# Kernel tuning notes

Hardware: AMD Instinct MI355X
Metric: run time of the kernel (lower is better)

The kernel has to match this reference:

```python
import jax, jax.numpy as jnp
import numpy as np

N = 20000   # nodes
E = 320000  # edges (before self-loops)
D = 128     # hidden_dim (= per-head out channels, concat=False)
H = 4       # heads
NEG_SLOPE = 0.2   # GATv2 leaky_relu default
LN_EPS = 1e-5


def setup_inputs() -> dict:
    key = jax.random.key(0)
    ks = jax.random.split(key, 12)
    s = 0.05
    w = lambda k, shp: (jax.random.normal(k, shp, jnp.float32) * s)
    return {
        "x": jax.random.normal(ks[0], (N, D), jnp.float32),
        "src": jax.random.randint(ks[1], (E,), 0, N, jnp.int32),
        "dst": jax.random.randint(ks[2], (E,), 0, N, jnp.int32),
        "Wl1": w(ks[3], (D, H * D)), "Wr1": w(ks[4], (D, H * D)),
        "att1": w(ks[5], (H, D)), "b1": jnp.zeros((D,), jnp.float32),
        "g1": jnp.ones((D,), jnp.float32), "be1": jnp.zeros((D,), jnp.float32),
        "Wl2": w(ks[6], (D, H * D)), "Wr2": w(ks[7], (D, H * D)),
        "att2": w(ks[8], (H, D)), "b2": jnp.zeros((D,), jnp.float32),
        "g2": jnp.ones((D,), jnp.float32), "be2": jnp.zeros((D,), jnp.float32),
    }


def gatv2_conv(x, src, dst, Wl, Wr, att, bias):
    """GATv2Conv with concat=False (mean over heads), share_weights=False."""
    n = x.shape[0]
    xl = (x @ Wl).reshape(n, H, D)  # source-side projection
    xr = (x @ Wr).reshape(n, H, D)  # target-side projection
    m = jax.nn.leaky_relu(xl[src] + xr[dst], NEG_SLOPE)     # [E', H, D]
    e = jnp.einsum('ehd,hd->eh', m, att)                     # [E', H]
    # segment softmax over edges grouped by destination node
    e_max = jax.ops.segment_max(e, dst, num_segments=n)      # [N, H]
    ex = jnp.exp(e - e_max[dst])
    denom = jax.ops.segment_sum(ex, dst, num_segments=n)     # [N, H]
    alpha = ex / (denom[dst] + 1e-16)                        # [E', H]
    out = jax.ops.segment_sum(alpha[:, :, None] * xl[src], dst, num_segments=n)
    return out.mean(axis=1) + bias                           # [N, D]


def layer_norm(x, g, b):
    mu = x.mean(axis=-1, keepdims=True)
    var = ((x - mu) ** 2).mean(axis=-1, keepdims=True)
    return (x - mu) * jax.lax.rsqrt(var + LN_EPS) * g + b


def reference(x, src, dst, Wl1, Wr1, att1, b1, g1, be1,
              Wl2, Wr2, att2, b2, g2, be2):
    n = x.shape[0]
    # PyG GATv2Conv default add_self_loops=True
    loops = jnp.arange(n, dtype=src.dtype)
    s = jnp.concatenate([src, loops])
    d = jnp.concatenate([dst, loops])

    h = gatv2_conv(x, s, d, Wl1, Wr1, att1, b1)
    h = layer_norm(h, g1, be1)
    h = jax.nn.relu(h + x)

    h2 = gatv2_conv(h, s, d, Wl2, Wr2, att2, b2)
    h2 = layer_norm(h2, g2, be2)
    return h2 + h
```

## Files before the change

kernel.cpp:

```cpp
#include <hip/hip_runtime.h>
#include <hip/hip_bf16.h>
#include <hip/hip_fp16.h>

#define NNODES 20000
#define MPAD   20480
#define NEDGES 320000
#define DIM    128
#define NH     4
#define ETOT   (NEDGES + NNODES)
#define LN_EPS 1e-5f

typedef unsigned char  u8;
typedef unsigned short u16;
typedef unsigned int   u32;

typedef _Float16    f16x2 __attribute__((ext_vector_type(2)));
typedef _Float16    f16x8 __attribute__((ext_vector_type(8)));
typedef float       f32x2 __attribute__((ext_vector_type(2)));
typedef float       f32x4 __attribute__((ext_vector_type(4)));
typedef signed char i8x8  __attribute__((ext_vector_type(8)));

__device__ inline u16 f2h(float f) {
    _Float16 h = (_Float16)f;
    union { _Float16 h; u16 u; } v; v.h = h; return v.u;
}
__device__ inline _Float16 bits2h(u16 b) {
    union { u16 u; _Float16 h; } v; v.u = b; return v.h;
}
__device__ inline f16x2 u2h2(u32 u) { union { u32 u; f16x2 h; } v; v.u = u; return v.h; }
__device__ inline u32 h22u(f16x2 h) { union { f16x2 h; u32 u; } v; v.h = h; return v.u; }
__device__ inline f16x2 habs2(f16x2 h) { return u2h2(h22u(h) & 0x7FFF7FFFu); }

#define GLDS16(g, l) __builtin_amdgcn_global_load_lds(                         \
    (const __attribute__((address_space(1))) void*)(g),                        \
    (__attribute__((address_space(3))) void*)(l), 16, 0, 0)


__global__ __launch_bounds__(256) void k_prep(const float* __restrict__ x, u16* __restrict__ xb,
                       const float* __restrict__ Wl1, const float* __restrict__ Wr1,
                       u16* __restrict__ Bt1,
                       const float* __restrict__ Wl2, const float* __restrict__ Wr2,
                       u16* __restrict__ Bt2,
                       int* __restrict__ deg) {
    const int b = blockIdx.x, t = threadIdx.x;
    const int gid = b * 256 + t;
    if (gid < NNODES) deg[gid] = 1;

    for (int j = gid; j < NNODES * 32; j += 256 * 256) {
        float4 v = ((const float4*)x)[j];
        ushort4 o;
        o.x = f2h(v.x); o.y = f2h(v.y); o.z = f2h(v.z); o.w = f2h(v.w);
        ((ushort4*)xb)[j] = o;
    }

    {
        const int m    = b >> 6;
        const int tile = b & 63;
        const int kt   = tile >> 4;
        const int nt   = tile & 15;
        const float* W = (m == 0) ? Wl1 : (m == 1) ? Wr1 : (m == 2) ? Wl2 : Wr2;
        u16* Bt        = (m < 2) ? Bt1 : Bt2;
        const int nbase = (m & 1) * 512 + nt * 32;

        __shared__ float lds[32][33];
        const int tx = t & 31, ty = t >> 5;
#pragma unroll
        for (int i = 0; i < 4; ++i) {
            int k = kt * 32 + ty + i * 8;
            lds[ty + i * 8][tx] = W[k * 512 + nt * 32 + tx];
        }
        __syncthreads();
#pragma unroll
        for (int i = 0; i < 4; ++i) {
            int nrow = nbase + ty + i * 8;
            Bt[nrow * 128 + kt * 32 + tx] = f2h(lds[tx][ty + i * 8]);
        }
    }
}


__global__ void k_hist(const int* __restrict__ dst, int* __restrict__ deg) {
    int i = blockIdx.x * blockDim.x + threadIdx.x;
    if (i < NEDGES) atomicAdd(&deg[dst[i]], 1);
}

__global__ __launch_bounds__(1024) void k_scan(const int* __restrict__ deg,
                                               int* __restrict__ row,
                                               int* __restrict__ cur) {
    __shared__ int part[1024];
    const int CH = 20;
    int t = threadIdx.x;
    int base = t * CH;
    int s = 0;
    int d[20];
    if (base < NNODES) {
#pragma unroll
        for (int q = 0; q < 5; ++q) {
            int4 v = ((const int4*)(deg + base))[q];
            d[q*4+0] = v.x; d[q*4+1] = v.y; d[q*4+2] = v.z; d[q*4+3] = v.w;
            s += v.x + v.y + v.z + v.w;
        }
    }
    part[t] = s;
    __syncthreads();
    for (int off = 1; off < 1024; off <<= 1) {
        int v = (t >= off) ? part[t - off] : 0;
        __syncthreads();
        part[t] += v;
        __syncthreads();
    }
    if (base < NNODES) {
        int run = (t == 0) ? 0 : part[t - 1];
#pragma unroll
        for (int i = 0; i < CH; i++) {
            row[base + i] = run; cur[base + i] = run; run += d[i];
        }
    }
    if (t == 1023) row[NNODES] = part[1023];
}

__global__ void k_scatter(const int* __restrict__ src, const int* __restrict__ dst,
                          int* __restrict__ col, int* __restrict__ cur) {
    int i = blockIdx.x * blockDim.x + threadIdx.x;
    if (i < NEDGES) {
        int d = dst[i];
        int pos = atomicAdd(&cur[d], 1);
        col[pos] = src[i];
    } else if (i < ETOT) {
        int n = i - NEDGES;
        int pos = atomicAdd(&cur[n], 1);
        col[pos] = n;
    }
}


__global__ __launch_bounds__(256, 2) void k_gemm_f16(const u16* __restrict__ A,
                                                     const u16* __restrict__ Bt,
                                                     u16* __restrict__ XL,
                                                     u16* __restrict__ XR) {
    __shared__ u16 smA[128 * 128];
    __shared__ u16 smB[128 * 128];
    const int L   = blockIdx.x;
    const int xcd = L & 7;
    const int w9  = L >> 3;
    const int bm  = (xcd * 20 + (w9 >> 3)) * 128;
    const int bn  = (w9 & 7) * 128;
    const int t  = threadIdx.x;
    const int w  = t >> 6;
    const int l  = t & 63;

    {
        char* smAb = (char*)smA;
        char* smBb = (char*)smB;
#pragma unroll
        for (int p = 0; p < 8; ++p) {
            int rbase = w * 32 + p * 4;
            int row   = rbase + (l >> 4);
            int j     = (l & 15) ^ (row & 7);
            const u16* ga = A  + (size_t)(bm + row) * 128 + j * 8;
            const u16* gb = Bt + (size_t)(bn + row) * 128 + j * 8;
            GLDS16(ga, smAb + rbase * 256);
            GLDS16(gb, smBb + rbase * 256);
        }
    }
    __syncthreads();

    const int wr  = (w >> 1) * 64;
    const int wc  = (w & 1) * 64;
    const int lr  = l & 15;
    const int lkb = (l >> 4) * 16;

    f32x4 acc[4][4] = {};

#pragma unroll
    for (int ks = 0; ks < 4; ++ks) {
        f16x8 af[4], bfr[4];
#pragma unroll
        for (int i = 0; i < 4; ++i) {
            int ra = wr + i * 16 + lr;
            af[i]  = *(const f16x8*)((const char*)smA +
                        ((ra * 256 + ks * 64 + lkb) ^ ((ra & 7) << 4)));
            int rb = wc + i * 16 + lr;
            bfr[i] = *(const f16x8*)((const char*)smB +
                        ((rb * 256 + ks * 64 + lkb) ^ ((rb & 7) << 4)));
        }
#pragma unroll
        for (int mi = 0; mi < 4; ++mi)
#pragma unroll
            for (int ni = 0; ni < 4; ++ni)
                acc[mi][ni] = __builtin_amdgcn_mfma_f32_16x16x32_f16(
                    bfr[ni], af[mi], acc[mi][ni], 0, 0, 0);
    }

    __syncthreads();
    u16* smC = smA;
    {
        const int n4 = (l >> 4) * 4;
#pragma unroll
        for (int mi = 0; mi < 4; ++mi) {
            int m = wr + mi * 16 + lr;
#pragma unroll
            for (int ni = 0; ni < 4; ++ni) {
                int n = wc + ni * 16 + n4;
                f32x4 v = acc[mi][ni];
                ushort4 o;
                o.x = f2h(v[0]); o.y = f2h(v[1]); o.z = f2h(v[2]); o.w = f2h(v[3]);
                *(ushort4*)((char*)smC + (m * 256 + ((n * 2) ^ ((m & 7) << 4)))) = o;
            }
        }
    }
    __syncthreads();
    {
        int r  = t >> 4;
        int cb = (t & 15) * 16;
        const bool left = (bn < 512);
        u16* base = left ? (XL + bn) : (XR + (bn - 512));
#pragma unroll
        for (int p = 0; p < 8; ++p) {
            int row = p * 16 + r;
            uint4 v = *(const uint4*)((const char*)smC +
                        (row * 256 + (cb ^ ((row & 7) << 4))));
            *(uint4*)(base + (size_t)(bm + row) * 512 + (cb >> 1)) = v;
        }
    }
}


__global__ __launch_bounds__(256) void k_quant(const u16* __restrict__ XL,
                                               u8* __restrict__ XLq,
                                               u16* __restrict__ scales) {
    const int wid = threadIdx.x >> 6;
    const int n   = blockIdx.x * 4 + wid;
    const int l   = threadIdx.x & 63;
    const int h   = l >> 4, e = l & 15;

    uint4 v = *(const uint4*)(XL + (size_t)n * 512 + h * 128 + e * 8);
    float vf[8];
    {
        f32x2 c;
        c = __builtin_convertvector(u2h2(v.x), f32x2); vf[0] = c[0]; vf[1] = c[1];
        c = __builtin_convertvector(u2h2(v.y), f32x2); vf[2] = c[0]; vf[3] = c[1];
        c = __builtin_convertvector(u2h2(v.z), f32x2); vf[4] = c[0]; vf[5] = c[1];
        c = __builtin_convertvector(u2h2(v.w), f32x2); vf[6] = c[0]; vf[7] = c[1];
    }
    float m = 0.f;
#pragma unroll
    for (int k = 0; k < 8; ++k) m = fmaxf(m, fabsf(vf[k]));
#pragma unroll
    for (int off = 1; off < 16; off <<= 1) m = fmaxf(m, __shfl_xor(m, off, 64));

    float scale = m * (1.f / 127.f);
    float inv   = (m > 0.f) ? (127.f / m) : 0.f;

    int q[8];
#pragma unroll
    for (int k = 0; k < 8; ++k) {
        int qi = (int)__builtin_rintf(vf[k] * inv);
        qi = qi > 127 ? 127 : (qi < -127 ? -127 : qi);
        q[k] = qi;
    }
    u32 lo = (q[0] & 255) | ((q[1] & 255) << 8) | ((q[2] & 255) << 16) | ((q[3] & 255) << 24);
    u32 hi = (q[4] & 255) | ((q[5] & 255) << 8) | ((q[6] & 255) << 16) | ((q[7] & 255) << 24);
    uint2 o; o.x = lo; o.y = hi;
    *(uint2*)(XLq + (size_t)n * 512 + h * 128 + e * 8) = o;
    if (e == 0) scales[n * 4 + h] = f2h(scale);
}


__global__ __launch_bounds__(256) void k_attn(const u8*  __restrict__ XLq,
                                              const u16* __restrict__ scales,
                                              const u16* __restrict__ XR,
                                              const float* __restrict__ att,
                                              const float* __restrict__ bias,
                                              const float* __restrict__ gamma,
                                              const float* __restrict__ beta,
                                              const int* __restrict__ row,
                                              const int* __restrict__ col,
                                              const float* __restrict__ res,
                                              float* __restrict__ out,
                                              u16* __restrict__ out_h,
                                              int relu_flag) {
    const int wid = __builtin_amdgcn_readfirstlane(threadIdx.x >> 6);
    const int n   = blockIdx.x * 4 + wid;
    const int l   = threadIdx.x & 63;
    const int h   = l >> 4;
    const int e   = l & 15;

    const f16x2 C06 = {(_Float16)0.6f, (_Float16)0.6f};
    const f16x2 C04 = {(_Float16)0.4f, (_Float16)0.4f};

    const int lane_off = h * 128 + e * 8;

    uint4 xru = *(const uint4*)(XR + (size_t)n * 512 + lane_off);
    f16x2 xr0 = u2h2(xru.x), xr1 = u2h2(xru.y), xr2 = u2h2(xru.z), xr3 = u2h2(xru.w);

    const float* ap = att + lane_off;
    float4 af0 = *(const float4*)(ap);
    float4 af1 = *(const float4*)(ap + 4);
    f16x2 at0 = {(_Float16)af0.x, (_Float16)af0.y};
    f16x2 at1 = {(_Float16)af0.z, (_Float16)af0.w};
    f16x2 at2 = {(_Float16)af1.x, (_Float16)af1.y};
    f16x2 at3 = {(_Float16)af1.z, (_Float16)af1.w};

    f16x2 acch[4] = {};
    float ssum = 0.f;

    const int beg = row[n], end = row[n + 1];

    for (int i = beg; i < end; i += 2) {
        int s0 = col[i];
        bool has2 = (i + 1 < end);
        int s1 = has2 ? col[i + 1] : s0;

        uint2 a0 = *(const uint2*)(XLq + (size_t)s0 * 512 + lane_off);
        uint2 a1 = *(const uint2*)(XLq + (size_t)s1 * 512 + lane_off);
        _Float16 sh0 = bits2h(scales[s0 * 4 + h]);
        _Float16 sh1 = bits2h(scales[s1 * 4 + h]);
        f16x2 s0h2 = {sh0, sh0};
        f16x2 s1h2 = {sh1, sh1};

        f16x8 q0, q1;
        {
            union { uint2 u; i8x8 c; } uc;
            uc.u = a0; q0 = __builtin_convertvector(uc.c, f16x8);
            uc.u = a1; q1 = __builtin_convertvector(uc.c, f16x8);
        }
        f16x2 q00 = __builtin_shufflevector(q0, q0, 0, 1);
        f16x2 q01 = __builtin_shufflevector(q0, q0, 2, 3);
        f16x2 q02 = __builtin_shufflevector(q0, q0, 4, 5);
        f16x2 q03 = __builtin_shufflevector(q0, q0, 6, 7);
        f16x2 q10 = __builtin_shufflevector(q1, q1, 0, 1);
        f16x2 q11 = __builtin_shufflevector(q1, q1, 2, 3);
        f16x2 q12 = __builtin_shufflevector(q1, q1, 4, 5);
        f16x2 q13 = __builtin_shufflevector(q1, q1, 6, 7);

        float e0, e1;
        {
            f16x2 v0 = q00 * s0h2 + xr0, v1 = q01 * s0h2 + xr1;
            f16x2 v2 = q02 * s0h2 + xr2, v3 = q03 * s0h2 + xr3;
            f16x2 k0 = v0 * C06 + habs2(v0) * C04;
            f16x2 k1 = v1 * C06 + habs2(v1) * C04;
            f16x2 k2 = v2 * C06 + habs2(v2) * C04;
            f16x2 k3 = v3 * C06 + habs2(v3) * C04;
            e0 = __builtin_amdgcn_fdot2(k0, at0, 0.f, false);
            e0 = __builtin_amdgcn_fdot2(k1, at1, e0, false);
            e0 = __builtin_amdgcn_fdot2(k2, at2, e0, false);
            e0 = __builtin_amdgcn_fdot2(k3, at3, e0, false);
        }
        {
            f16x2 v0 = q10 * s1h2 + xr0, v1 = q11 * s1h2 + xr1;
            f16x2 v2 = q12 * s1h2 + xr2, v3 = q13 * s1h2 + xr3;
            f16x2 k0 = v0 * C06 + habs2(v0) * C04;
            f16x2 k1 = v1 * C06 + habs2(v1) * C04;
            f16x2 k2 = v2 * C06 + habs2(v2) * C04;
            f16x2 k3 = v3 * C06 + habs2(v3) * C04;
            e1 = __builtin_amdgcn_fdot2(k0, at0, 0.f, false);
            e1 = __builtin_amdgcn_fdot2(k1, at1, e1, false);
            e1 = __builtin_amdgcn_fdot2(k2, at2, e1, false);
            e1 = __builtin_amdgcn_fdot2(k3, at3, e1, false);
        }

#pragma unroll
        for (int m = 1; m < 16; m <<= 1) {
            e0 += __shfl_xor(e0, m, 64);
            e1 += __shfl_xor(e1, m, 64);
        }

        float p0 = __expf(e0);
        float p1 = has2 ? __expf(e1) : 0.f;
        ssum += p0 + p1;

        _Float16 ph0s = (_Float16)(p0 * (float)sh0);
        _Float16 ph1s = (_Float16)(p1 * (float)sh1);
        f16x2 ph0 = {ph0s, ph0s};
        f16x2 ph1 = {ph1s, ph1s};
        acch[0] = acch[0] + ph0 * q00 + ph1 * q10;
        acch[1] = acch[1] + ph0 * q01 + ph1 * q11;
        acch[2] = acch[2] + ph0 * q02 + ph1 * q12;
        acch[3] = acch[3] + ph0 * q03 + ph1 * q13;
    }

    float acc[8];
    {
        f32x2 c;
        c = __builtin_convertvector(acch[0], f32x2); acc[0] = c[0]; acc[1] = c[1];
        c = __builtin_convertvector(acch[1], f32x2); acc[2] = c[0]; acc[3] = c[1];
        c = __builtin_convertvector(acch[2], f32x2); acc[4] = c[0]; acc[5] = c[1];
        c = __builtin_convertvector(acch[3], f32x2); acc[6] = c[0]; acc[7] = c[1];
    }
    float inv = 1.f / (ssum + 1e-16f);
#pragma unroll
    for (int jj = 0; jj < 8; ++jj) acc[jj] *= inv;
#pragma unroll
    for (int jj = 0; jj < 8; ++jj) acc[jj] += __shfl_xor(acc[jj], 16, 64);
#pragma unroll
    for (int jj = 0; jj < 8; ++jj) acc[jj] += __shfl_xor(acc[jj], 32, 64);

    if (h == 0) {
        const int dd = e * 8;
        float4 b40 = *(const float4*)(bias + dd);
        float4 b41 = *(const float4*)(bias + dd + 4);
        float y[8];
        y[0] = acc[0]*0.25f + b40.x; y[1] = acc[1]*0.25f + b40.y;
        y[2] = acc[2]*0.25f + b40.z; y[3] = acc[3]*0.25f + b40.w;
        y[4] = acc[4]*0.25f + b41.x; y[5] = acc[5]*0.25f + b41.y;
        y[6] = acc[6]*0.25f + b41.z; y[7] = acc[7]*0.25f + b41.w;

        float s1 = 0.f, s2 = 0.f;
#pragma unroll
        for (int jj = 0; jj < 8; ++jj) { s1 += y[jj]; s2 += y[jj]*y[jj]; }
#pragma unroll
        for (int m = 1; m < 16; m <<= 1) {
            s1 += __shfl_xor(s1, m, 64);
            s2 += __shfl_xor(s2, m, 64);
        }
        float mu = s1 * (1.f / 128.f);
        float var = s2 * (1.f / 128.f) - mu * mu;
        float rstd = rsqrtf(var + LN_EPS);

        float4 g40 = *(const float4*)(gamma + dd);
        float4 g41 = *(const float4*)(gamma + dd + 4);
        float4 e40 = *(const float4*)(beta + dd);
        float4 e41 = *(const float4*)(beta + dd + 4);
        float4 r40 = *(const float4*)(res + (size_t)n * 128 + dd);
        float4 r41 = *(const float4*)(res + (size_t)n * 128 + dd + 4);
        float g[8] = {g40.x,g40.y,g40.z,g40.w,g41.x,g41.y,g41.z,g41.w};
        float be[8] = {e40.x,e40.y,e40.z,e40.w,e41.x,e41.y,e41.z,e41.w};
        float r[8] = {r40.x,r40.y,r40.z,r40.w,r41.x,r41.y,r41.z,r41.w};
#pragma unroll
        for (int jj = 0; jj < 8; ++jj) {
            y[jj] = (y[jj] - mu) * rstd * g[jj] + be[jj] + r[jj];
            if (relu_flag) y[jj] = fmaxf(y[jj], 0.f);
        }
        float4 o0 = {y[0],y[1],y[2],y[3]};
        float4 o1 = {y[4],y[5],y[6],y[7]};
        *(float4*)(out + (size_t)n * 128 + dd)     = o0;
        *(float4*)(out + (size_t)n * 128 + dd + 4) = o1;
        if (out_h) {
            ushort4 oh0, oh1;
            oh0.x = f2h(y[0]); oh0.y = f2h(y[1]); oh0.z = f2h(y[2]); oh0.w = f2h(y[3]);
            oh1.x = f2h(y[4]); oh1.y = f2h(y[5]); oh1.z = f2h(y[6]); oh1.w = f2h(y[7]);
            *(ushort4*)(out_h + (size_t)n * 128 + dd)     = oh0;
            *(ushort4*)(out_h + (size_t)n * 128 + dd + 4) = oh1;
        }
    }
}


extern "C" void kernel_launch(void* const* d_in, const int* in_sizes, int n_in,
                              void* d_out, int out_size, void* d_ws, size_t ws_size,
                              hipStream_t stream) {
    const float* x    = (const float*)d_in[0];
    const int*   src  = (const int*)d_in[1];
    const int*   dst  = (const int*)d_in[2];
    const float* Wl1  = (const float*)d_in[3];
    const float* Wr1  = (const float*)d_in[4];
    const float* att1 = (const float*)d_in[5];
    const float* b1   = (const float*)d_in[6];
    const float* g1   = (const float*)d_in[7];
    const float* be1  = (const float*)d_in[8];
    const float* Wl2  = (const float*)d_in[9];
    const float* Wr2  = (const float*)d_in[10];
    const float* att2 = (const float*)d_in[11];
    const float* b2   = (const float*)d_in[12];
    const float* g2   = (const float*)d_in[13];
    const float* be2  = (const float*)d_in[14];
    float* out = (float*)d_out;

    char* ws = (char*)d_ws;
    size_t off = 0;
    u16*   xlb  = (u16*)(ws + off);   off += (size_t)MPAD * 512 * 2;
    u16*   xrb  = (u16*)(ws + off);   off += (size_t)MPAD * 512 * 2;
    u8*    xlq  = (u8*)(ws + off);    off += (size_t)NNODES * 512;
    u16*   scl  = (u16*)(ws + off);   off += (size_t)NNODES * 4 * 2;
    u16*   xb   = (u16*)(ws + off);   off += (size_t)MPAD * 128 * 2;
    float* hbuf = (float*)(ws + off); off += (size_t)NNODES * 128 * 4;
    u16*   Bt1  = (u16*)(ws + off);   off += (size_t)1024 * 128 * 2;
    u16*   Bt2  = (u16*)(ws + off);   off += (size_t)1024 * 128 * 2;
    int*   deg  = (int*)(ws + off);   off += (size_t)NNODES * 4;
    int*   rowp = (int*)(ws + off);   off += (size_t)(NNODES + 1) * 4;
    int*   cur  = (int*)(ws + off);   off += (size_t)NNODES * 4;
    int*   col  = (int*)(ws + off);   off += (size_t)ETOT * 4;

    k_prep<<<256, 256, 0, stream>>>(x, xb, Wl1, Wr1, Bt1, Wl2, Wr2, Bt2, deg);
    k_hist<<<(NEDGES + 255) / 256, 256, 0, stream>>>(dst, deg);
    k_scan<<<1, 1024, 0, stream>>>(deg, rowp, cur);
    k_scatter<<<(ETOT + 255) / 256, 256, 0, stream>>>(src, dst, col, cur);

    k_gemm_f16<<<MPAD / 128 * 8, 256, 0, stream>>>(xb, Bt1, xlb, xrb);
    k_quant<<<NNODES / 4, 256, 0, stream>>>(xlb, xlq, scl);
    k_attn<<<NNODES / 4, 256, 0, stream>>>(xlq, scl, xrb, att1, b1, g1, be1, rowp, col,
                                           x, hbuf, xb, 1);
    k_gemm_f16<<<MPAD / 128 * 8, 256, 0, stream>>>(xb, Bt2, xlb, xrb);
    k_quant<<<NNODES / 4, 256, 0, stream>>>(xlb, xlq, scl);
    k_attn<<<NNODES / 4, 256, 0, stream>>>(xlq, scl, xrb, att2, b2, g2, be2, rowp, col,
                                           hbuf, out, (u16*)nullptr, 0);
}
```

Measured before the change: 190.8 us.

## Fuse int8 quantization of XL into GEMM epilogue and use byte-perm int8-to-fp16 decode

The separate quantization kernel is removed. The GEMM epilogue now quantizes the XL half of each tile straight from shared memory to int8 with per-head scales, so the fp16 XL buffer is never written to or read back from global memory. The attention kernel also replaces the int8-to-fp16 vector conversion with a magic-number trick: a byte permute into 0x64xx halves followed by a subtract of 1152. This removes two launches and about 40MB of traffic, but adds register and ALU pressure to the GEMM epilogue.

```diff
diff --git a/kernel.cpp b/kernel.cpp
--- a/kernel.cpp
+++ b/kernel.cpp
@@ -18,7 +18,6 @@
 typedef _Float16    f16x8 __attribute__((ext_vector_type(8)));
 typedef float       f32x2 __attribute__((ext_vector_type(2)));
 typedef float       f32x4 __attribute__((ext_vector_type(4)));
-typedef signed char i8x8  __attribute__((ext_vector_type(8)));
 
 __device__ inline u16 f2h(float f) {
     _Float16 h = (_Float16)f;
@@ -136,7 +135,8 @@
 
 __global__ __launch_bounds__(256, 2) void k_gemm_f16(const u16* __restrict__ A,
                                                      const u16* __restrict__ Bt,
-                                                     u16* __restrict__ XL,
+                                                     u8*  __restrict__ XLq,
+                                                     u16* __restrict__ scales,
                                                      u16* __restrict__ XR) {
     __shared__ u16 smA[128 * 128];
     __shared__ u16 smB[128 * 128];
@@ -210,11 +210,43 @@
         }
     }
     __syncthreads();
-    {
+
+    if (bn < 512) {
+        const int head = bn >> 7;
+        const int lr16 = l & 15;
+        const int rg   = l >> 4;
+#pragma unroll
+        for (int p = 0; p < 8; ++p) {
+            int r = w * 32 + p * 4 + rg;
+            uint4 vv = *(const uint4*)((const char*)smC +
+                        (r * 256 + ((lr16 * 16) ^ ((r & 7) << 4))));
+            f32x2 c0 = __builtin_convertvector(u2h2(vv.x), f32x2);
+            f32x2 c1 = __builtin_convertvector(u2h2(vv.y), f32x2);
+            f32x2 c2 = __builtin_convertvector(u2h2(vv.z), f32x2);
+            f32x2 c3 = __builtin_convertvector(u2h2(vv.w), f32x2);
+            float f[8] = {c0[0],c0[1],c1[0],c1[1],c2[0],c2[1],c3[0],c3[1]};
+            float m = 0.f;
+#pragma unroll
+            for (int k = 0; k < 8; ++k) m = fmaxf(m, fabsf(f[k]));
+#pragma unroll
+            for (int o = 1; o < 16; o <<= 1) m = fmaxf(m, __shfl_xor(m, o, 64));
+            float inv = (m > 0.f) ? (127.f / m) : 0.f;
+            int q[8];
+#pragma unroll
+            for (int k = 0; k < 8; ++k) {
+                int qi = (int)__builtin_rintf(f[k] * inv);
+                q[k] = qi > 127 ? 127 : (qi < -127 ? -127 : qi);
+            }
+            u32 lo = (q[0]&255) | ((q[1]&255)<<8) | ((q[2]&255)<<16) | ((q[3]&255)<<24);
+            u32 hi = (q[4]&255) | ((q[5]&255)<<8) | ((q[6]&255)<<16) | ((q[7]&255)<<24);
+            uint2 pk; pk.x = lo; pk.y = hi;
+            *(uint2*)(XLq + (size_t)(bm + r) * 512 + head * 128 + lr16 * 8) = pk;
+            if (lr16 == 0) scales[(bm + r) * 4 + head] = f2h(m * (1.f / 127.f));
+        }
+    } else {
         int r  = t >> 4;
         int cb = (t & 15) * 16;
-        const bool left = (bn < 512);
-        u16* base = left ? (XL + bn) : (XR + (bn - 512));
+        u16* base = XR + (bn - 512);
 #pragma unroll
         for (int p = 0; p < 8; ++p) {
             int row = p * 16 + r;
@@ -223,47 +255,6 @@
             *(uint4*)(base + (size_t)(bm + row) * 512 + (cb >> 1)) = v;
         }
     }
-}
-
-
-__global__ __launch_bounds__(256) void k_quant(const u16* __restrict__ XL,
-                                               u8* __restrict__ XLq,
-                                               u16* __restrict__ scales) {
-    const int wid = threadIdx.x >> 6;
-    const int n   = blockIdx.x * 4 + wid;
-    const int l   = threadIdx.x & 63;
-    const int h   = l >> 4, e = l & 15;
-
-    uint4 v = *(const uint4*)(XL + (size_t)n * 512 + h * 128 + e * 8);
-    float vf[8];
-    {
-        f32x2 c;
-        c = __builtin_convertvector(u2h2(v.x), f32x2); vf[0] = c[0]; vf[1] = c[1];
-        c = __builtin_convertvector(u2h2(v.y), f32x2); vf[2] = c[0]; vf[3] = c[1];
-        c = __builtin_convertvector(u2h2(v.z), f32x2); vf[4] = c[0]; vf[5] = c[1];
-        c = __builtin_convertvector(u2h2(v.w), f32x2); vf[6] = c[0]; vf[7] = c[1];
-    }
-    float m = 0.f;
-#pragma unroll
-    for (int k = 0; k < 8; ++k) m = fmaxf(m, fabsf(vf[k]));
-#pragma unroll
-    for (int off = 1; off < 16; off <<= 1) m = fmaxf(m, __shfl_xor(m, off, 64));
-
-    float scale = m * (1.f / 127.f);
-    float inv   = (m > 0.f) ? (127.f / m) : 0.f;
-
-    int q[8];
-#pragma unroll
-    for (int k = 0; k < 8; ++k) {
-        int qi = (int)__builtin_rintf(vf[k] * inv);
-        qi = qi > 127 ? 127 : (qi < -127 ? -127 : qi);
-        q[k] = qi;
-    }
-    u32 lo = (q[0] & 255) | ((q[1] & 255) << 8) | ((q[2] & 255) << 16) | ((q[3] & 255) << 24);
-    u32 hi = (q[4] & 255) | ((q[5] & 255) << 8) | ((q[6] & 255) << 16) | ((q[7] & 255) << 24);
-    uint2 o; o.x = lo; o.y = hi;
-    *(uint2*)(XLq + (size_t)n * 512 + h * 128 + e * 8) = o;
-    if (e == 0) scales[n * 4 + h] = f2h(scale);
 }
 
 
@@ -288,6 +279,8 @@
 
     const f16x2 C06 = {(_Float16)0.6f, (_Float16)0.6f};
     const f16x2 C04 = {(_Float16)0.4f, (_Float16)0.4f};
+    const f16x2 M1152 = {(_Float16)(-1152.f), (_Float16)(-1152.f)};
+    const u32 K64 = 0x64646464u;
 
     const int lane_off = h * 128 + e * 8;
 
@@ -319,20 +312,16 @@
         f16x2 s0h2 = {sh0, sh0};
         f16x2 s1h2 = {sh1, sh1};
 
-        f16x8 q0, q1;
-        {
-            union { uint2 u; i8x8 c; } uc;
-            uc.u = a0; q0 = __builtin_convertvector(uc.c, f16x8);
-            uc.u = a1; q1 = __builtin_convertvector(uc.c, f16x8);
-        }
-        f16x2 q00 = __builtin_shufflevector(q0, q0, 0, 1);
-        f16x2 q01 = __builtin_shufflevector(q0, q0, 2, 3);
-        f16x2 q02 = __builtin_shufflevector(q0, q0, 4, 5);
-        f16x2 q03 = __builtin_shufflevector(q0, q0, 6, 7);
-        f16x2 q10 = __builtin_shufflevector(q1, q1, 0, 1);
-        f16x2 q11 = __builtin_shufflevector(q1, q1, 2, 3);
-        f16x2 q12 = __builtin_shufflevector(q1, q1, 4, 5);
-        f16x2 q13 = __builtin_shufflevector(q1, q1, 6, 7);
+        u32 w00 = a0.x ^ 0x80808080u, w01 = a0.y ^ 0x80808080u;
+        u32 w10 = a1.x ^ 0x80808080u, w11 = a1.y ^ 0x80808080u;
+        f16x2 q00 = u2h2(__builtin_amdgcn_perm(K64, w00, 0x04010400u)) + M1152;
+        f16x2 q01 = u2h2(__builtin_amdgcn_perm(K64, w00, 0x04030402u)) + M1152;
+        f16x2 q02 = u2h2(__builtin_amdgcn_perm(K64, w01, 0x04010400u)) + M1152;
+        f16x2 q03 = u2h2(__builtin_amdgcn_perm(K64, w01, 0x04030402u)) + M1152;
+        f16x2 q10 = u2h2(__builtin_amdgcn_perm(K64, w10, 0x04010400u)) + M1152;
+        f16x2 q11 = u2h2(__builtin_amdgcn_perm(K64, w10, 0x04030402u)) + M1152;
+        f16x2 q12 = u2h2(__builtin_amdgcn_perm(K64, w11, 0x04010400u)) + M1152;
+        f16x2 q13 = u2h2(__builtin_amdgcn_perm(K64, w11, 0x04030402u)) + M1152;
 
         float e0, e1;
         {
@@ -469,10 +458,9 @@
 
     char* ws = (char*)d_ws;
     size_t off = 0;
-    u16*   xlb  = (u16*)(ws + off);   off += (size_t)MPAD * 512 * 2;
+    u8*    xlq  = (u8*)(ws + off);    off += (size_t)MPAD * 512;
+    u16*   scl  = (u16*)(ws + off);   off += (size_t)MPAD * 4 * 2;
     u16*   xrb  = (u16*)(ws + off);   off += (size_t)MPAD * 512 * 2;
-    u8*    xlq  = (u8*)(ws + off);    off += (size_t)NNODES * 512;
-    u16*   scl  = (u16*)(ws + off);   off += (size_t)NNODES * 4 * 2;
     u16*   xb   = (u16*)(ws + off);   off += (size_t)MPAD * 128 * 2;
     float* hbuf = (float*)(ws + off); off += (size_t)NNODES * 128 * 4;
     u16*   Bt1  = (u16*)(ws + off);   off += (size_t)1024 * 128 * 2;
@@ -487,12 +475,10 @@
     k_scan<<<1, 1024, 0, stream>>>(deg, rowp, cur);
     k_scatter<<<(ETOT + 255) / 256, 256, 0, stream>>>(src, dst, col, cur);
 
-    k_gemm_f16<<<MPAD / 128 * 8, 256, 0, stream>>>(xb, Bt1, xlb, xrb);
-    k_quant<<<NNODES / 4, 256, 0, stream>>>(xlb, xlq, scl);
+    k_gemm_f16<<<MPAD / 128 * 8, 256, 0, stream>>>(xb, Bt1, xlq, scl, xrb);
     k_attn<<<NNODES / 4, 256, 0, stream>>>(xlq, scl, xrb, att1, b1, g1, be1, rowp, col,
                                            x, hbuf, xb, 1);
-    k_gemm_f16<<<MPAD / 128 * 8, 256, 0, stream>>>(xb, Bt2, xlb, xrb);
-    k_quant<<<NNODES / 4, 256, 0, stream>>>(xlb, xlq, scl);
+    k_gemm_f16<<<MPAD / 128 * 8, 256, 0, stream>>>(xb, Bt2, xlq, scl, xrb);
     k_attn<<<NNODES / 4, 256, 0, stream>>>(xlq, scl, xrb, att2, b2, g2, be2, rowp, col,
                                            hbuf, out, (u16*)nullptr, 0);
 }
```

Result: faster. 180.4 us (-5.4%).
